# Kernel optimization log

Hardware: AMD Instinct MI355X
Metric: run time of the kernel (lower is better)

## Reference

```python
import jax, jax.numpy as jnp
import numpy as np

B, T, D, H, O = 32768, 96, 7, 3, 7

def setup_inputs() -> dict:
    key = jax.random.key(0)
    ks = jax.random.split(key, 7)
    s_ih = 1.0 / np.sqrt(H)
    inp = {
        "x": jax.random.normal(ks[0], (B, T, D), dtype=jnp.float32),
        # PyTorch nn.LSTM params (gate order i,f,g,o), uniform(-1/sqrt(H), 1/sqrt(H))
        "W_ih": jax.random.uniform(ks[1], (4 * H, D), jnp.float32, -s_ih, s_ih),
        "W_hh": jax.random.uniform(ks[2], (4 * H, H), jnp.float32, -s_ih, s_ih),
        "b_ih": jax.random.uniform(ks[3], (4 * H,), jnp.float32, -s_ih, s_ih),
        "b_hh": jax.random.uniform(ks[4], (4 * H,), jnp.float32, -s_ih, s_ih),
        # nn.Linear(H*T, O*T): weight [out,in]
        "W_lin": jax.random.uniform(ks[5], (O * T, H * T), jnp.float32, -1.0 / np.sqrt(H * T), 1.0 / np.sqrt(H * T)),
        "b_lin": jax.random.uniform(ks[6], (O * T,), jnp.float32, -1.0 / np.sqrt(H * T), 1.0 / np.sqrt(H * T)),
    }
    return inp

def _lstm(x, W_ih, W_hh, b_ih, b_hh):
    b = x.shape[0]
    h0 = jnp.zeros((b, H), x.dtype)
    c0 = jnp.zeros((b, H), x.dtype)
    bias = b_ih + b_hh

    def step(carry, x_t):
        h, c = carry
        gates = x_t @ W_ih.T + h @ W_hh.T + bias  # [b, 4H]
        i, f, g, o = jnp.split(gates, 4, axis=-1)
        i = jax.nn.sigmoid(i)
        f = jax.nn.sigmoid(f)
        g = jnp.tanh(g)
        o = jax.nn.sigmoid(o)
        c = f * c + i * g
        h = o * jnp.tanh(c)
        return (h, c), h

    (_, _), hs = jax.lax.scan(step, (h0, c0), jnp.swapaxes(x, 0, 1))  # hs: [T, b, H]
    return jnp.swapaxes(hs, 0, 1)  # [b, T, H]

def reference(x, W_ih, W_hh, b_ih, b_hh, W_lin, b_lin):
    out = _lstm(x, W_ih, W_hh, b_ih, b_hh)            # [B, T, H]
    out = out.reshape(x.shape[0], -1)                  # [B, T*H]
    out = out @ W_lin.T + b_lin                        # [B, O*T]
    return out.reshape(x.shape)                        # [B, T, D]
```

## Files before the change

kernel.cpp:

```cpp
#include <hip/hip_runtime.h>
#include <stdint.h>

typedef unsigned short u16;
typedef unsigned int u32;
typedef __attribute__((ext_vector_type(8))) __bf16 bf16x8;
typedef __attribute__((ext_vector_type(4))) float f32x4;

#define B_TOT   32768
#define T_SEQ   96
#define D_IN    7
#define K_LIN   288
#define N_LIN   672
#define N_PAD   768

#define LOG2E      1.4426950408889634f
#define TWO_LOG2E  2.8853900817779268f

__device__ __forceinline__ u16 f2bf(float f) {
  u32 u = __builtin_bit_cast(u32, f);
  u += 0x7fffu + ((u >> 16) & 1u);
  return (u16)(u >> 16);
}
__device__ __forceinline__ float sig2(float zp) {
  return __builtin_amdgcn_rcpf(1.0f + __builtin_amdgcn_exp2f(-zp));
}
__device__ __forceinline__ float tanh2(float zpp) {
  return 1.0f - 2.0f * __builtin_amdgcn_rcpf(1.0f + __builtin_amdgcn_exp2f(zpp));
}
template<int Q>
__device__ __forceinline__ float qbcast(float v) {
  int i = __builtin_bit_cast(int, v);
  i = __builtin_amdgcn_update_dpp(0, i, Q * 0x55, 0xF, 0xF, true);
  return __builtin_bit_cast(float, i);
}

__global__ __launch_bounds__(256) void convert_kernel(
    const float* __restrict__ Wlin, const float* __restrict__ blin,
    u16* __restrict__ Bw, float* __restrict__ biasp)
{
  int i = blockIdx.x * 256 + threadIdx.x;
  if (i < N_PAD * K_LIN) {
    int n = i / K_LIN;
    int kk = i - n * K_LIN;
    int jm = kk / T_SEQ;
    int tm = kk - jm * T_SEQ;
    Bw[i] = f2bf((n < N_LIN) ? Wlin[n * K_LIN + tm * 3 + jm] : 0.0f);
  }
  if (i < N_PAD) biasp[i] = (i < N_LIN) ? blin[i] : 0.0f;
}

__device__ __forceinline__ void steps8(
    const float* __restrict__ xc,
    float& h0, float& h1, float& h2, float& c,
    const float (&wih)[4][7], const float (&whh)[4][3], const float (&bias)[4],
    float* hv8)
{
#pragma unroll
  for (int s = 0; s < 8; ++s) {
    float zi = bias[0], zf = bias[1], zg = bias[2], zo = bias[3];
#pragma unroll
    for (int k = 0; k < 7; ++k) {
      const float xv = xc[s * 7 + k];
      zi = fmaf(xv, wih[0][k], zi);
      zf = fmaf(xv, wih[1][k], zf);
      zg = fmaf(xv, wih[2][k], zg);
      zo = fmaf(xv, wih[3][k], zo);
    }
    zi = fmaf(h2, whh[0][2], fmaf(h1, whh[0][1], fmaf(h0, whh[0][0], zi)));
    zf = fmaf(h2, whh[1][2], fmaf(h1, whh[1][1], fmaf(h0, whh[1][0], zf)));
    zg = fmaf(h2, whh[2][2], fmaf(h1, whh[2][1], fmaf(h0, whh[2][0], zg)));
    zo = fmaf(h2, whh[3][2], fmaf(h1, whh[3][1], fmaf(h0, whh[3][0], zo)));
    float ig = sig2(zi);
    float fg = sig2(zf);
    float gg = tanh2(zg);
    float og = sig2(zo);
    c = fmaf(fg, c, ig * gg);
    float hv = og * tanh2(c * TWO_LOG2E);
    hv8[s] = hv;
    h0 = qbcast<0>(hv);
    h1 = qbcast<1>(hv);
    h2 = qbcast<2>(hv);
  }
}

__global__ __launch_bounds__(256) void lstm_kernel(
    const float* __restrict__ x,
    const float* __restrict__ Wih, const float* __restrict__ Whh,
    const float* __restrict__ bih, const float* __restrict__ bhh,
    u16* __restrict__ hs)
{
  __shared__ float sW[132];
  __shared__ __align__(16) float xb[2][64 * 56];

  const int tid = threadIdx.x;
  for (int i = tid; i < 132; i += 256) {
    float v; int row;
    if (i < 84)       { v = Wih[i];       row = i / 7; }
    else if (i < 120) { v = Whh[i - 84];  row = (i - 84) / 3; }
    else              { v = bih[i - 120] + bhh[i - 120]; row = i - 120; }
    const int G = row / 3;
    sW[i] = v * ((G == 2) ? TWO_LOG2E : LOG2E);
  }
  __syncthreads();

  const int j  = tid & 3;
  const int jj = (j < 3) ? j : 2;

  float wih[4][7], whh[4][3], bias[4];
#pragma unroll
  for (int G = 0; G < 4; ++G) {
    const int row = G * 3 + jj;
#pragma unroll
    for (int k = 0; k < 7; ++k) wih[G][k] = sW[row * 7 + k];
#pragma unroll
    for (int m = 0; m < 3; ++m) whh[G][m] = sW[84 + row * 3 + m];
    bias[G] = sW[120 + row];
  }
#pragma unroll
  for (int G = 0; G < 4; ++G) {
#pragma unroll
    for (int k = 0; k < 7; ++k) asm volatile("" : "+v"(wih[G][k]));
#pragma unroll
    for (int m = 0; m < 3; ++m) asm volatile("" : "+v"(whh[G][m]));
    asm volatile("" : "+v"(bias[G]));
  }

  const int cs = tid & 63;
  const int w  = tid >> 6;
  const int b0 = blockIdx.x * 64;
  const float* gbase = x + (size_t)(b0 + cs) * (T_SEQ * D_IN) + w * 4;

  const int cc = tid >> 2;
  const float* xc0 = &xb[0][cc * 56];
  const float* xc1 = &xb[1][cc * 56];
  float* xw0 = &xb[0][cs * 56 + w * 4];
  float* xw1 = &xb[1][cs * 56 + w * 4];

  const int b = b0 + cc;
  u16* __restrict__ hrow = hs + (size_t)b * K_LIN + jj * T_SEQ;

  float h0 = 0.f, h1 = 0.f, h2 = 0.f, c = 0.f;
  float hv8[8];

  {
    const float4* gp = (const float4*)gbase;
    float4 g0 = gp[0], g1 = gp[4], g2 = gp[8];
    float4 g3 = {};
    if (w < 2) g3 = gp[12];
    float4* ld = (float4*)xw0;
    ld[0] = g0; ld[4] = g1; ld[8] = g2;
    if (w < 2) ld[12] = g3;
  }
  __syncthreads();

#pragma unroll 1
  for (int n2 = 0; n2 < 6; ++n2) {
    const int n = n2 * 2;
    {
      const float4* gp = (const float4*)(gbase + (n + 1) * 56);
      float4 g0 = gp[0], g1 = gp[4], g2 = gp[8];
      float4 g3 = {};
      if (w < 2) g3 = gp[12];
      steps8(xc0, h0, h1, h2, c, wih, whh, bias, hv8);
      __builtin_amdgcn_sched_barrier(0);
      {
        float4* ld = (float4*)xw1;
        ld[0] = g0; ld[4] = g1; ld[8] = g2;
        if (w < 2) ld[12] = g3;
      }
      if (j < 3) {
        u32 w0_, w1_, w2_, w3_;
        asm("v_cvt_pk_bf16_f32 %0, %1, %2" : "=v"(w0_) : "v"(hv8[0]), "v"(hv8[1]));
        asm("v_cvt_pk_bf16_f32 %0, %1, %2" : "=v"(w1_) : "v"(hv8[2]), "v"(hv8[3]));
        asm("v_cvt_pk_bf16_f32 %0, %1, %2" : "=v"(w2_) : "v"(hv8[4]), "v"(hv8[5]));
        asm("v_cvt_pk_bf16_f32 %0, %1, %2" : "=v"(w3_) : "v"(hv8[6]), "v"(hv8[7]));
        uint4 pkv; pkv.x = w0_; pkv.y = w1_; pkv.z = w2_; pkv.w = w3_;
        *(uint4*)(hrow + n * 8) = pkv;
      }
      __syncthreads();
    }
    {
      const bool has_next = (n2 < 5);
      float4 g0 = {}, g1 = {}, g2 = {}, g3 = {};
      if (has_next) {
        const float4* gp = (const float4*)(gbase + (n + 2) * 56);
        g0 = gp[0]; g1 = gp[4]; g2 = gp[8];
        if (w < 2) g3 = gp[12];
      }
      steps8(xc1, h0, h1, h2, c, wih, whh, bias, hv8);
      __builtin_amdgcn_sched_barrier(0);
      if (has_next) {
        float4* ld = (float4*)xw0;
        ld[0] = g0; ld[4] = g1; ld[8] = g2;
        if (w < 2) ld[12] = g3;
      }
      if (j < 3) {
        u32 w0_, w1_, w2_, w3_;
        asm("v_cvt_pk_bf16_f32 %0, %1, %2" : "=v"(w0_) : "v"(hv8[0]), "v"(hv8[1]));
        asm("v_cvt_pk_bf16_f32 %0, %1, %2" : "=v"(w1_) : "v"(hv8[2]), "v"(hv8[3]));
        asm("v_cvt_pk_bf16_f32 %0, %1, %2" : "=v"(w2_) : "v"(hv8[4]), "v"(hv8[5]));
        asm("v_cvt_pk_bf16_f32 %0, %1, %2" : "=v"(w3_) : "v"(hv8[6]), "v"(hv8[7]));
        uint4 pkv; pkv.x = w0_; pkv.y = w1_; pkv.z = w2_; pkv.w = w3_;
        *(uint4*)(hrow + (n + 1) * 8) = pkv;
      }
      __syncthreads();
    }
  }
}

__device__ __forceinline__ void gload16(const u16* g, u16* l) {
  __builtin_amdgcn_global_load_lds(
      (const __attribute__((address_space(1))) void*)g,
      (__attribute__((address_space(3))) void*)l, 16, 0, 0);
}

__global__ __launch_bounds__(256) void gemm_kernel(
    const u16* __restrict__ A, const u16* __restrict__ Bw,
    const float* __restrict__ bias, float* __restrict__ C)
{
  __shared__ u16 As[128 * 32];
  __shared__ u16 Bs[128 * 32];
  const int tid  = threadIdx.x;
  const int lane = tid & 63;
  const int wid  = tid >> 6;
  const int wm = wid >> 1, wn = wid & 1;

  int bx = blockIdx.x;
  int swz = (bx & 7) * 192 + (bx >> 3);
  const int bm = swz / 6;
  const int bn = swz - bm * 6;
  const size_t m0 = (size_t)bm * 128;
  const int n0 = bn * 128;

  const int ra = tid >> 2;
  const int ca = (tid & 3) * 8;
  const u16* ga = A  + (m0 + (size_t)ra) * K_LIN + ca;
  const u16* gb = Bw + (size_t)(n0 + ra) * K_LIN + ca;
  u16* lA = &As[wid * 512];
  u16* lB = &Bs[wid * 512];

  const int l15 = lane & 15, l4 = lane >> 4;
  const u16* pAf = &As[(wm * 64 + l15) * 32 + l4 * 8];
  const u16* pBf = &Bs[(wn * 64 + l15) * 32 + l4 * 8];

  f32x4 acc[4][4] = {};

  for (int kt = 0; kt < 9; ++kt) {
    const int ko = kt * 32;
    gload16(ga + ko,               lA);
    gload16(ga + 64 * K_LIN + ko,  lA + 2048);
    gload16(gb + ko,               lB);
    gload16(gb + 64 * K_LIN + ko,  lB + 2048);
    __syncthreads();
    bf16x8 af[4], bfv[4];
#pragma unroll
    for (int i = 0; i < 4; ++i) af[i]  = *(const bf16x8*)(const void*)(pAf + i * 512);
#pragma unroll
    for (int i = 0; i < 4; ++i) bfv[i] = *(const bf16x8*)(const void*)(pBf + i * 512);
#pragma unroll
    for (int mi = 0; mi < 4; ++mi)
#pragma unroll
      for (int ni = 0; ni < 4; ++ni)
        acc[mi][ni] = __builtin_amdgcn_mfma_f32_16x16x32_bf16(af[mi], bfv[ni], acc[mi][ni], 0, 0, 0);
    __syncthreads();
  }

  float bv[4];
#pragma unroll
  for (int ni = 0; ni < 4; ++ni) bv[ni] = bias[n0 + wn * 64 + ni * 16 + l15];

#pragma unroll
  for (int mi = 0; mi < 4; ++mi) {
#pragma unroll
    for (int ni = 0; ni < 4; ++ni) {
      const int col = n0 + wn * 64 + ni * 16 + l15;
      if (col < N_LIN) {
#pragma unroll
        for (int r = 0; r < 4; ++r) {
          const size_t row = m0 + wm * 64 + mi * 16 + l4 * 4 + r;
          C[row * N_LIN + col] = acc[mi][ni][r] + bv[ni];
        }
      }
    }
  }
}

extern "C" void kernel_launch(void* const* d_in, const int* in_sizes, int n_in,
                              void* d_out, int out_size, void* d_ws, size_t ws_size,
                              hipStream_t stream) {
  const float* x    = (const float*)d_in[0];
  const float* Wih  = (const float*)d_in[1];
  const float* Whh  = (const float*)d_in[2];
  const float* bih  = (const float*)d_in[3];
  const float* bhh  = (const float*)d_in[4];
  const float* Wlin = (const float*)d_in[5];
  const float* blin = (const float*)d_in[6];
  float* out = (float*)d_out;

  u16* hs = (u16*)d_ws;
  u16* Bw = (u16*)((char*)d_ws + (size_t)B_TOT * K_LIN * 2);
  float* biasp = (float*)((char*)d_ws + (size_t)B_TOT * K_LIN * 2 + (size_t)N_PAD * K_LIN * 2);

  convert_kernel<<<(N_PAD * K_LIN + 255) / 256, 256, 0, stream>>>(Wlin, blin, Bw, biasp);
  lstm_kernel<<<B_TOT / 64, 256, 0, stream>>>(x, Wih, Whh, bih, bhh, hs);
  gemm_kernel<<<(B_TOT / 128) * (N_PAD / 128), 256, 0, stream>>>(hs, Bw, biasp, out);
}
```

Before: 70.33 us.

## Fuse LSTM recurrence and output linear layer into one kernel via LDS

Merges the LSTM kernel and the bf16 MFMA GEMM into a single kernel. Each block keeps its 64 rows of hidden states in padded LDS and then multiplies them by the linear weights, which are read directly from global memory. This removes the global round-trip of the hidden-state matrix and one kernel launch. In exchange the x double buffer becomes a single buffer with an extra barrier per chunk, LDS use per block rises, and B-operand reuse across blocks now depends on L2.

```diff
diff --git a/kernel.cpp b/kernel.cpp
--- a/kernel.cpp
+++ b/kernel.cpp
@@ -12,6 +12,7 @@
 #define K_LIN   288
 #define N_LIN   672
 #define N_PAD   768
+#define HS_LD   296
 
 #define LOG2E      1.4426950408889634f
 #define TWO_LOG2E  2.8853900817779268f
@@ -83,16 +84,18 @@
   }
 }
 
-__global__ __launch_bounds__(256) void lstm_kernel(
+__global__ __launch_bounds__(256) void fused_kernel(
     const float* __restrict__ x,
     const float* __restrict__ Wih, const float* __restrict__ Whh,
     const float* __restrict__ bih, const float* __restrict__ bhh,
-    u16* __restrict__ hs)
+    const u16* __restrict__ Bw, const float* __restrict__ biasp,
+    float* __restrict__ C)
 {
   __shared__ float sW[132];
-  __shared__ __align__(16) float xb[2][64 * 56];
-
+  __shared__ __align__(16) float xbuf[64 * 56];
+  __shared__ __align__(16) u16  hs_lds[64 * HS_LD];
   const int tid = threadIdx.x;
+
   for (int i = tid; i < 132; i += 256) {
     float v; int row;
     if (i < 84)       { v = Wih[i];       row = i / 7; }
@@ -129,15 +132,11 @@
   const int w  = tid >> 6;
   const int b0 = blockIdx.x * 64;
   const float* gbase = x + (size_t)(b0 + cs) * (T_SEQ * D_IN) + w * 4;
+  float* xw = &xbuf[cs * 56 + w * 4];
 
   const int cc = tid >> 2;
-  const float* xc0 = &xb[0][cc * 56];
-  const float* xc1 = &xb[1][cc * 56];
-  float* xw0 = &xb[0][cs * 56 + w * 4];
-  float* xw1 = &xb[1][cs * 56 + w * 4];
-
-  const int b = b0 + cc;
-  u16* __restrict__ hrow = hs + (size_t)b * K_LIN + jj * T_SEQ;
+  const float* xc = &xbuf[cc * 56];
+  u16* hlrow = &hs_lds[cc * HS_LD + jj * T_SEQ];
 
   float h0 = 0.f, h1 = 0.f, h2 = 0.f, c = 0.f;
   float hv8[8];
@@ -147,138 +146,74 @@
     float4 g0 = gp[0], g1 = gp[4], g2 = gp[8];
     float4 g3 = {};
     if (w < 2) g3 = gp[12];
-    float4* ld = (float4*)xw0;
+    float4* ld = (float4*)xw;
     ld[0] = g0; ld[4] = g1; ld[8] = g2;
     if (w < 2) ld[12] = g3;
   }
   __syncthreads();
 
 #pragma unroll 1
-  for (int n2 = 0; n2 < 6; ++n2) {
-    const int n = n2 * 2;
-    {
+  for (int n = 0; n < 12; ++n) {
+    const bool has_next = (n < 11);
+    float4 g0 = {}, g1 = {}, g2 = {}, g3 = {};
+    if (has_next) {
       const float4* gp = (const float4*)(gbase + (n + 1) * 56);
-      float4 g0 = gp[0], g1 = gp[4], g2 = gp[8];
-      float4 g3 = {};
+      g0 = gp[0]; g1 = gp[4]; g2 = gp[8];
       if (w < 2) g3 = gp[12];
-      steps8(xc0, h0, h1, h2, c, wih, whh, bias, hv8);
-      __builtin_amdgcn_sched_barrier(0);
-      {
-        float4* ld = (float4*)xw1;
-        ld[0] = g0; ld[4] = g1; ld[8] = g2;
-        if (w < 2) ld[12] = g3;
+    }
+    steps8(xc, h0, h1, h2, c, wih, whh, bias, hv8);
+    if (j < 3) {
+      u32 w0_, w1_, w2_, w3_;
+      asm("v_cvt_pk_bf16_f32 %0, %1, %2" : "=v"(w0_) : "v"(hv8[0]), "v"(hv8[1]));
+      asm("v_cvt_pk_bf16_f32 %0, %1, %2" : "=v"(w1_) : "v"(hv8[2]), "v"(hv8[3]));
+      asm("v_cvt_pk_bf16_f32 %0, %1, %2" : "=v"(w2_) : "v"(hv8[4]), "v"(hv8[5]));
+      asm("v_cvt_pk_bf16_f32 %0, %1, %2" : "=v"(w3_) : "v"(hv8[6]), "v"(hv8[7]));
+      uint4 pkv; pkv.x = w0_; pkv.y = w1_; pkv.z = w2_; pkv.w = w3_;
+      *(uint4*)(hlrow + n * 8) = pkv;
+    }
+    __syncthreads();
+    if (has_next) {
+      float4* ld = (float4*)xw;
+      ld[0] = g0; ld[4] = g1; ld[8] = g2;
+      if (w < 2) ld[12] = g3;
+      __syncthreads();
+    }
+  }
+
+  const int lane = tid & 63;
+  const int l15 = lane & 15, l4 = lane >> 4;
+  const int wid = tid >> 6;
+
+#pragma unroll 1
+  for (int p = 0; p < 4; ++p) {
+    const int n0 = wid * 192 + p * 48;
+    f32x4 acc[4][3] = {};
+#pragma unroll
+    for (int kt = 0; kt < 9; ++kt) {
+      bf16x8 af[4];
+#pragma unroll
+      for (int mt = 0; mt < 4; ++mt)
+        af[mt] = *(const bf16x8*)(const void*)&hs_lds[(mt * 16 + l15) * HS_LD + kt * 32 + l4 * 8];
+#pragma unroll
+      for (int nt = 0; nt < 3; ++nt) {
+        bf16x8 bfr = *(const bf16x8*)(const void*)(Bw + (size_t)(n0 + nt * 16 + l15) * K_LIN + kt * 32 + l4 * 8);
+#pragma unroll
+        for (int mt = 0; mt < 4; ++mt)
+          acc[mt][nt] = __builtin_amdgcn_mfma_f32_16x16x32_bf16(af[mt], bfr, acc[mt][nt], 0, 0, 0);
       }
-      if (j < 3) {
-        u32 w0_, w1_, w2_, w3_;
-        asm("v_cvt_pk_bf16_f32 %0, %1, %2" : "=v"(w0_) : "v"(hv8[0]), "v"(hv8[1]));
-        asm("v_cvt_pk_bf16_f32 %0, %1, %2" : "=v"(w1_) : "v"(hv8[2]), "v"(hv8[3]));
-        asm("v_cvt_pk_bf16_f32 %0, %1, %2" : "=v"(w2_) : "v"(hv8[4]), "v"(hv8[5]));
-        asm("v_cvt_pk_bf16_f32 %0, %1, %2" : "=v"(w3_) : "v"(hv8[6]), "v"(hv8[7]));
-        uint4 pkv; pkv.x = w0_; pkv.y = w1_; pkv.z = w2_; pkv.w = w3_;
-        *(uint4*)(hrow + n * 8) = pkv;
-      }
-      __syncthreads();
-    }
-    {
-      const bool has_next = (n2 < 5);
-      float4 g0 = {}, g1 = {}, g2 = {}, g3 = {};
-      if (has_next) {
-        const float4* gp = (const float4*)(gbase + (n + 2) * 56);
-        g0 = gp[0]; g1 = gp[4]; g2 = gp[8];
-        if (w < 2) g3 = gp[12];
-      }
-      steps8(xc1, h0, h1, h2, c, wih, whh, bias, hv8);
-      __builtin_amdgcn_sched_barrier(0);
-      if (has_next) {
-        float4* ld = (float4*)xw0;
-        ld[0] = g0; ld[4] = g1; ld[8] = g2;
-        if (w < 2) ld[12] = g3;
-      }
-      if (j < 3) {
-        u32 w0_, w1_, w2_, w3_;
-        asm("v_cvt_pk_bf16_f32 %0, %1, %2" : "=v"(w0_) : "v"(hv8[0]), "v"(hv8[1]));
-        asm("v_cvt_pk_bf16_f32 %0, %1, %2" : "=v"(w1_) : "v"(hv8[2]), "v"(hv8[3]));
-        asm("v_cvt_pk_bf16_f32 %0, %1, %2" : "=v"(w2_) : "v"(hv8[4]), "v"(hv8[5]));
-        asm("v_cvt_pk_bf16_f32 %0, %1, %2" : "=v"(w3_) : "v"(hv8[6]), "v"(hv8[7]));
-        uint4 pkv; pkv.x = w0_; pkv.y = w1_; pkv.z = w2_; pkv.w = w3_;
-        *(uint4*)(hrow + (n + 1) * 8) = pkv;
-      }
-      __syncthreads();
-    }
-  }
-}
-
-__device__ __forceinline__ void gload16(const u16* g, u16* l) {
-  __builtin_amdgcn_global_load_lds(
-      (const __attribute__((address_space(1))) void*)g,
-      (__attribute__((address_space(3))) void*)l, 16, 0, 0);
-}
-
-__global__ __launch_bounds__(256) void gemm_kernel(
-    const u16* __restrict__ A, const u16* __restrict__ Bw,
-    const float* __restrict__ bias, float* __restrict__ C)
-{
-  __shared__ u16 As[128 * 32];
-  __shared__ u16 Bs[128 * 32];
-  const int tid  = threadIdx.x;
-  const int lane = tid & 63;
-  const int wid  = tid >> 6;
-  const int wm = wid >> 1, wn = wid & 1;
-
-  int bx = blockIdx.x;
-  int swz = (bx & 7) * 192 + (bx >> 3);
-  const int bm = swz / 6;
-  const int bn = swz - bm * 6;
-  const size_t m0 = (size_t)bm * 128;
-  const int n0 = bn * 128;
-
-  const int ra = tid >> 2;
-  const int ca = (tid & 3) * 8;
-  const u16* ga = A  + (m0 + (size_t)ra) * K_LIN + ca;
-  const u16* gb = Bw + (size_t)(n0 + ra) * K_LIN + ca;
-  u16* lA = &As[wid * 512];
-  u16* lB = &Bs[wid * 512];
-
-  const int l15 = lane & 15, l4 = lane >> 4;
-  const u16* pAf = &As[(wm * 64 + l15) * 32 + l4 * 8];
-  const u16* pBf = &Bs[(wn * 64 + l15) * 32 + l4 * 8];
-
-  f32x4 acc[4][4] = {};
-
-  for (int kt = 0; kt < 9; ++kt) {
-    const int ko = kt * 32;
-    gload16(ga + ko,               lA);
-    gload16(ga + 64 * K_LIN + ko,  lA + 2048);
-    gload16(gb + ko,               lB);
-    gload16(gb + 64 * K_LIN + ko,  lB + 2048);
-    __syncthreads();
-    bf16x8 af[4], bfv[4];
-#pragma unroll
-    for (int i = 0; i < 4; ++i) af[i]  = *(const bf16x8*)(const void*)(pAf + i * 512);
-#pragma unroll
-    for (int i = 0; i < 4; ++i) bfv[i] = *(const bf16x8*)(const void*)(pBf + i * 512);
-#pragma unroll
-    for (int mi = 0; mi < 4; ++mi)
-#pragma unroll
-      for (int ni = 0; ni < 4; ++ni)
-        acc[mi][ni] = __builtin_amdgcn_mfma_f32_16x16x32_bf16(af[mi], bfv[ni], acc[mi][ni], 0, 0, 0);
-    __syncthreads();
-  }
-
-  float bv[4];
-#pragma unroll
-  for (int ni = 0; ni < 4; ++ni) bv[ni] = bias[n0 + wn * 64 + ni * 16 + l15];
-
-#pragma unroll
-  for (int mi = 0; mi < 4; ++mi) {
-#pragma unroll
-    for (int ni = 0; ni < 4; ++ni) {
-      const int col = n0 + wn * 64 + ni * 16 + l15;
+    }
+#pragma unroll
+    for (int nt = 0; nt < 3; ++nt) {
+      const int col = n0 + nt * 16 + l15;
       if (col < N_LIN) {
-#pragma unroll
-        for (int r = 0; r < 4; ++r) {
-          const size_t row = m0 + wm * 64 + mi * 16 + l4 * 4 + r;
-          C[row * N_LIN + col] = acc[mi][ni][r] + bv[ni];
+        const float bv = biasp[col];
+#pragma unroll
+        for (int mt = 0; mt < 4; ++mt) {
+#pragma unroll
+          for (int r = 0; r < 4; ++r) {
+            const size_t row = (size_t)(b0 + mt * 16 + l4 * 4 + r);
+            C[row * N_LIN + col] = acc[mt][nt][r] + bv;
+          }
         }
       }
     }
@@ -297,11 +232,9 @@
   const float* blin = (const float*)d_in[6];
   float* out = (float*)d_out;
 
-  u16* hs = (u16*)d_ws;
-  u16* Bw = (u16*)((char*)d_ws + (size_t)B_TOT * K_LIN * 2);
-  float* biasp = (float*)((char*)d_ws + (size_t)B_TOT * K_LIN * 2 + (size_t)N_PAD * K_LIN * 2);
+  u16* Bw = (u16*)d_ws;
+  float* biasp = (float*)((char*)d_ws + (size_t)N_PAD * K_LIN * 2);
 
   convert_kernel<<<(N_PAD * K_LIN + 255) / 256, 256, 0, stream>>>(Wlin, blin, Bw, biasp);
-  lstm_kernel<<<B_TOT / 64, 256, 0, stream>>>(x, Wih, Whh, bih, bhh, hs);
-  gemm_kernel<<<(B_TOT / 128) * (N_PAD / 128), 256, 0, stream>>>(hs, Bw, biasp, out);
-}
+  fused_kernel<<<B_TOT / 64, 256, 0, stream>>>(x, Wih, Whh, bih, bhh, Bw, biasp, out);
+}
```

Result: slower. 125.1 us (+77.9%).

## Spread LSTM gates across 16 lanes per sequence with swizzle exchange

Applied to the files above, without the earlier changes.

Each batch element now uses 16 lanes, one per gate row, instead of 4 lanes each computing all four gates. Gate activations are unified into a single sigmoid with a per-lane affine select, and hidden states are exchanged with ds_swizzle while gate values are gathered with DPP broadcasts. Blocks process 16 sequences with smaller staging buffers, and launch bounds request higher occupancy. This shortens the per-step dependent chain but multiplies total lane work and cross-lane traffic.

```diff
diff --git a/kernel.cpp b/kernel.cpp
--- a/kernel.cpp
+++ b/kernel.cpp
@@ -21,16 +21,16 @@
   u += 0x7fffu + ((u >> 16) & 1u);
   return (u16)(u >> 16);
 }
-__device__ __forceinline__ float sig2(float zp) {
-  return __builtin_amdgcn_rcpf(1.0f + __builtin_amdgcn_exp2f(-zp));
-}
-__device__ __forceinline__ float tanh2(float zpp) {
-  return 1.0f - 2.0f * __builtin_amdgcn_rcpf(1.0f + __builtin_amdgcn_exp2f(zpp));
-}
 template<int Q>
 __device__ __forceinline__ float qbcast(float v) {
   int i = __builtin_bit_cast(int, v);
   i = __builtin_amdgcn_update_dpp(0, i, Q * 0x55, 0xF, 0xF, true);
+  return __builtin_bit_cast(float, i);
+}
+template<int PAT>
+__device__ __forceinline__ float swz(float v) {
+  int i = __builtin_bit_cast(int, v);
+  i = __builtin_amdgcn_ds_swizzle(i, PAT);
   return __builtin_bit_cast(float, i);
 }
 
@@ -49,48 +49,46 @@
   if (i < N_PAD) biasp[i] = (i < N_LIN) ? blin[i] : 0.0f;
 }
 
-__device__ __forceinline__ void steps8(
+__device__ __forceinline__ void steps8_gp(
     const float* __restrict__ xc,
-    float& h0, float& h1, float& h2, float& c,
-    const float (&wih)[4][7], const float (&whh)[4][3], const float (&bias)[4],
-    float* hv8)
+    float& h, float& c,
+    const float (&wih)[7], const float (&whs)[4], float bias,
+    float sel_s, float sel_b, float* hv8)
 {
 #pragma unroll
   for (int s = 0; s < 8; ++s) {
-    float zi = bias[0], zf = bias[1], zg = bias[2], zo = bias[3];
-#pragma unroll
-    for (int k = 0; k < 7; ++k) {
-      const float xv = xc[s * 7 + k];
-      zi = fmaf(xv, wih[0][k], zi);
-      zf = fmaf(xv, wih[1][k], zf);
-      zg = fmaf(xv, wih[2][k], zg);
-      zo = fmaf(xv, wih[3][k], zo);
-    }
-    zi = fmaf(h2, whh[0][2], fmaf(h1, whh[0][1], fmaf(h0, whh[0][0], zi)));
-    zf = fmaf(h2, whh[1][2], fmaf(h1, whh[1][1], fmaf(h0, whh[1][0], zf)));
-    zg = fmaf(h2, whh[2][2], fmaf(h1, whh[2][1], fmaf(h0, whh[2][0], zg)));
-    zo = fmaf(h2, whh[3][2], fmaf(h1, whh[3][1], fmaf(h0, whh[3][0], zo)));
-    float ig = sig2(zi);
-    float fg = sig2(zf);
-    float gg = tanh2(zg);
-    float og = sig2(zo);
-    c = fmaf(fg, c, ig * gg);
-    float hv = og * tanh2(c * TWO_LOG2E);
+    float z = bias;
+#pragma unroll
+    for (int k = 0; k < 7; ++k) z = fmaf(xc[s * 7 + k], wih[k], z);
+    float r1 = swz<0x101F>(h);
+    float r2 = swz<0x201F>(h);
+    float r3 = swz<0x301F>(h);
+    z = fmaf(h,  whs[0], z);
+    z = fmaf(r1, whs[1], z);
+    z = fmaf(r2, whs[2], z);
+    z = fmaf(r3, whs[3], z);
+    float sg = __builtin_amdgcn_rcpf(1.0f + __builtin_amdgcn_exp2f(z));
+    float a = fmaf(sel_s, sg, sel_b);
+    float ai = qbcast<0>(a);
+    float af = qbcast<1>(a);
+    float ag = qbcast<2>(a);
+    float ao = qbcast<3>(a);
+    c = fmaf(af, c, ai * ag);
+    float t = 1.0f - 2.0f * __builtin_amdgcn_rcpf(1.0f + __builtin_amdgcn_exp2f(c * TWO_LOG2E));
+    float hv = ao * t;
     hv8[s] = hv;
-    h0 = qbcast<0>(hv);
-    h1 = qbcast<1>(hv);
-    h2 = qbcast<2>(hv);
-  }
-}
-
-__global__ __launch_bounds__(256) void lstm_kernel(
+    h = hv;
+  }
+}
+
+__global__ __launch_bounds__(256, 8) void lstm_kernel(
     const float* __restrict__ x,
     const float* __restrict__ Wih, const float* __restrict__ Whh,
     const float* __restrict__ bih, const float* __restrict__ bhh,
     u16* __restrict__ hs)
 {
   __shared__ float sW[132];
-  __shared__ __align__(16) float xb[2][64 * 56];
+  __shared__ __align__(16) float xb[2][16 * 56];
 
   const int tid = threadIdx.x;
   for (int i = tid; i < 132; i += 256) {
@@ -99,76 +97,64 @@
     else if (i < 120) { v = Whh[i - 84];  row = (i - 84) / 3; }
     else              { v = bih[i - 120] + bhh[i - 120]; row = i - 120; }
     const int G = row / 3;
-    sW[i] = v * ((G == 2) ? TWO_LOG2E : LOG2E);
+    sW[i] = v * ((G == 2) ? -TWO_LOG2E : -LOG2E);
   }
   __syncthreads();
 
-  const int j  = tid & 3;
-  const int jj = (j < 3) ? j : 2;
-
-  float wih[4][7], whh[4][3], bias[4];
-#pragma unroll
-  for (int G = 0; G < 4; ++G) {
-    const int row = G * 3 + jj;
-#pragma unroll
-    for (int k = 0; k < 7; ++k) wih[G][k] = sW[row * 7 + k];
-#pragma unroll
-    for (int m = 0; m < 3; ++m) whh[G][m] = sW[84 + row * 3 + m];
-    bias[G] = sW[120 + row];
-  }
-#pragma unroll
-  for (int G = 0; G < 4; ++G) {
-#pragma unroll
-    for (int k = 0; k < 7; ++k) asm volatile("" : "+v"(wih[G][k]));
-#pragma unroll
-    for (int m = 0; m < 3; ++m) asm volatile("" : "+v"(whh[G][m]));
-    asm volatile("" : "+v"(bias[G]));
-  }
-
-  const int cs = tid & 63;
-  const int w  = tid >> 6;
-  const int b0 = blockIdx.x * 64;
-  const float* gbase = x + (size_t)(b0 + cs) * (T_SEQ * D_IN) + w * 4;
-
-  const int cc = tid >> 2;
+  const int sub = tid & 15;
+  const int g   = sub & 3;
+  const int q   = sub >> 2;
+  const int jj  = (q < 3) ? q : 2;
+  const int row = g * 3 + jj;
+
+  float wih[7], whs[4];
+#pragma unroll
+  for (int k = 0; k < 7; ++k) wih[k] = sW[row * 7 + k];
+  float bias = sW[120 + row];
+#pragma unroll
+  for (int r = 0; r < 4; ++r) {
+    const int su = q ^ r;
+    whs[r] = (su < 3) ? sW[84 + row * 3 + su] : 0.0f;
+  }
+  const float sel_s = (g == 2) ? 2.0f : 1.0f;
+  const float sel_b = (g == 2) ? -1.0f : 0.0f;
+#pragma unroll
+  for (int k = 0; k < 7; ++k) asm volatile("" : "+v"(wih[k]));
+#pragma unroll
+  for (int r = 0; r < 4; ++r) asm volatile("" : "+v"(whs[r]));
+  asm volatile("" : "+v"(bias));
+
+  const int b0 = blockIdx.x * 16;
+  const bool stager = (tid < 224);
+  const int sch = tid / 14;
+  const int sof = (tid % 14) * 4;
+  const float* gbase = x + (size_t)(b0 + sch) * (T_SEQ * D_IN) + sof;
+  float* xw0 = &xb[0][tid * 4];
+  float* xw1 = &xb[1][tid * 4];
+
+  const int cc = tid >> 4;
   const float* xc0 = &xb[0][cc * 56];
   const float* xc1 = &xb[1][cc * 56];
-  float* xw0 = &xb[0][cs * 56 + w * 4];
-  float* xw1 = &xb[1][cs * 56 + w * 4];
-
-  const int b = b0 + cc;
-  u16* __restrict__ hrow = hs + (size_t)b * K_LIN + jj * T_SEQ;
-
-  float h0 = 0.f, h1 = 0.f, h2 = 0.f, c = 0.f;
+
+  u16* __restrict__ hrow = hs + (size_t)(b0 + cc) * K_LIN + jj * T_SEQ;
+  const bool writer = (g == 0) && (q < 3);
+
+  float h = 0.f, c = 0.f;
   float hv8[8];
 
-  {
-    const float4* gp = (const float4*)gbase;
-    float4 g0 = gp[0], g1 = gp[4], g2 = gp[8];
-    float4 g3 = {};
-    if (w < 2) g3 = gp[12];
-    float4* ld = (float4*)xw0;
-    ld[0] = g0; ld[4] = g1; ld[8] = g2;
-    if (w < 2) ld[12] = g3;
-  }
+  if (stager) *(float4*)xw0 = *(const float4*)gbase;
   __syncthreads();
 
 #pragma unroll 1
   for (int n2 = 0; n2 < 6; ++n2) {
     const int n = n2 * 2;
     {
-      const float4* gp = (const float4*)(gbase + (n + 1) * 56);
-      float4 g0 = gp[0], g1 = gp[4], g2 = gp[8];
-      float4 g3 = {};
-      if (w < 2) g3 = gp[12];
-      steps8(xc0, h0, h1, h2, c, wih, whh, bias, hv8);
+      float4 gpre = {};
+      if (stager) gpre = *(const float4*)(gbase + (n + 1) * 56);
+      steps8_gp(xc0, h, c, wih, whs, bias, sel_s, sel_b, hv8);
       __builtin_amdgcn_sched_barrier(0);
-      {
-        float4* ld = (float4*)xw1;
-        ld[0] = g0; ld[4] = g1; ld[8] = g2;
-        if (w < 2) ld[12] = g3;
-      }
-      if (j < 3) {
+      if (stager) *(float4*)xw1 = gpre;
+      if (writer) {
         u32 w0_, w1_, w2_, w3_;
         asm("v_cvt_pk_bf16_f32 %0, %1, %2" : "=v"(w0_) : "v"(hv8[0]), "v"(hv8[1]));
         asm("v_cvt_pk_bf16_f32 %0, %1, %2" : "=v"(w1_) : "v"(hv8[2]), "v"(hv8[3]));
@@ -180,21 +166,13 @@
       __syncthreads();
     }
     {
-      const bool has_next = (n2 < 5);
-      float4 g0 = {}, g1 = {}, g2 = {}, g3 = {};
-      if (has_next) {
-        const float4* gp = (const float4*)(gbase + (n + 2) * 56);
-        g0 = gp[0]; g1 = gp[4]; g2 = gp[8];
-        if (w < 2) g3 = gp[12];
-      }
-      steps8(xc1, h0, h1, h2, c, wih, whh, bias, hv8);
+      const bool hn = (n2 < 5);
+      float4 gpre = {};
+      if (stager && hn) gpre = *(const float4*)(gbase + (n + 2) * 56);
+      steps8_gp(xc1, h, c, wih, whs, bias, sel_s, sel_b, hv8);
       __builtin_amdgcn_sched_barrier(0);
-      if (has_next) {
-        float4* ld = (float4*)xw0;
-        ld[0] = g0; ld[4] = g1; ld[8] = g2;
-        if (w < 2) ld[12] = g3;
-      }
-      if (j < 3) {
+      if (stager && hn) *(float4*)xw0 = gpre;
+      if (writer) {
         u32 w0_, w1_, w2_, w3_;
         asm("v_cvt_pk_bf16_f32 %0, %1, %2" : "=v"(w0_) : "v"(hv8[0]), "v"(hv8[1]));
         asm("v_cvt_pk_bf16_f32 %0, %1, %2" : "=v"(w1_) : "v"(hv8[2]), "v"(hv8[3]));
@@ -226,9 +204,9 @@
   const int wm = wid >> 1, wn = wid & 1;
 
   int bx = blockIdx.x;
-  int swz = (bx & 7) * 192 + (bx >> 3);
-  const int bm = swz / 6;
-  const int bn = swz - bm * 6;
+  int swzb = (bx & 7) * 192 + (bx >> 3);
+  const int bm = swzb / 6;
+  const int bn = swzb - bm * 6;
   const size_t m0 = (size_t)bm * 128;
   const int n0 = bn * 128;
 
@@ -302,6 +280,6 @@
   float* biasp = (float*)((char*)d_ws + (size_t)B_TOT * K_LIN * 2 + (size_t)N_PAD * K_LIN * 2);
 
   convert_kernel<<<(N_PAD * K_LIN + 255) / 256, 256, 0, stream>>>(Wlin, blin, Bw, biasp);
-  lstm_kernel<<<B_TOT / 64, 256, 0, stream>>>(x, Wih, Whh, bih, bhh, hs);
+  lstm_kernel<<<B_TOT / 16, 256, 0, stream>>>(x, Wih, Whh, bih, bhh, hs);
   gemm_kernel<<<(B_TOT / 128) * (N_PAD / 128), 256, 0, stream>>>(hs, Bw, biasp, out);
 }
```

Measured after the change: 83.19 us. +18.3%, slower.
